# Kernel optimization log

Measured on AMD Instinct MI355X. Metric: run time of the kernel, lower is better.

The kernel has to match this reference:

```python
import jax, jax.numpy as jnp
import numpy as np

N_NODES = 100000
N_EDGES = 800000
N_FEAT = 64
H_DIM = 64
N_GRAPHS = 64


def _glorot(key, fan_in, fan_out):
    lim = np.sqrt(6.0 / (fan_in + fan_out)).astype(np.float32)
    return jax.random.uniform(key, (fan_in, fan_out), jnp.float32, -lim, lim)


def setup_inputs() -> dict:
    key = jax.random.key(0)
    ks = jax.random.split(key, 10)
    x = jax.random.normal(ks[0], (N_NODES, N_FEAT), jnp.float32)
    edge_index = jax.random.randint(ks[1], (2, N_EDGES), 0, N_NODES, dtype=jnp.int64)
    batch = jnp.sort(jax.random.randint(ks[2], (N_NODES,), 0, N_GRAPHS, dtype=jnp.int64))
    return {
        "x": x,
        "edge_index": edge_index,
        "batch": batch,
        "W0": _glorot(ks[3], N_FEAT, H_DIM), "b0": jnp.zeros((H_DIM,), jnp.float32),
        "W1": _glorot(ks[4], H_DIM, H_DIM), "b1": jnp.zeros((H_DIM,), jnp.float32),
        "W2": _glorot(ks[5], H_DIM, H_DIM), "b2": jnp.zeros((H_DIM,), jnp.float32),
        "Wl": _glorot(ks[6], H_DIM, H_DIM),
        "bl": jax.random.normal(ks[7], (H_DIM,), jnp.float32) * 0.01,
    }


def _gcn_conv(h, W, b, row, col, dinv_r, dinv_c, n_nodes):
    # PyG GCNConv: x W, then sym-normalized aggregation over edges+self-loops
    h = h @ W                                   # [N, H]
    msg = h[row] * (dinv_r * dinv_c)[:, None]   # gather + scale, [E+N, H]
    out = jax.ops.segment_sum(msg, col, num_segments=n_nodes)  # scatter-add
    return out + b


def reference(x, edge_index, batch, W0, b0, W1, b1, W2, b2, Wl, bl):
    n = x.shape[0]
    loops = jnp.arange(n, dtype=edge_index.dtype)
    row = jnp.concatenate([edge_index[0], loops])  # source nodes (+self-loops)
    col = jnp.concatenate([edge_index[1], loops])  # destination nodes
    deg = jax.ops.segment_sum(jnp.ones_like(col, dtype=x.dtype), col, num_segments=n)
    dinv = jnp.where(deg > 0, jax.lax.rsqrt(deg), 0.0)
    dinv_r, dinv_c = dinv[row], dinv[col]

    out = x
    for W, b in ((W0, b0), (W1, b1), (W2, b2)):
        out = jax.nn.relu(_gcn_conv(out, W, b, row, col, dinv_r, dinv_c, n))
        # F.dropout(training=False) is identity in eval mode
    return (out, out @ Wl + bl)
```

## Files before the change

### kernel.cpp

```cpp
#include <hip/hip_runtime.h>

#define NN 100000
#define NE 800000
#define HD 64
#define BK 128
#define NBUCK ((NN + BK - 1) / BK)
#define PA_EPT 16
#define PA_NB ((NE + 256 * PA_EPT - 1) / (256 * PA_EPT))
#define LDW 68

__device__ __forceinline__ int load_idx(const void* ei, int i, bool is32) {
    if (is32) return ((const int*)ei)[i];
    return (int)(((const long long*)ei)[i]);
}

__device__ __forceinline__ unsigned short f2bf(float f) {
    unsigned u = __float_as_uint(f);
    return (unsigned short)((u + 0x7FFFu + ((u >> 16) & 1u)) >> 16);
}

__device__ __forceinline__ void bfacc(const uint4& u, float4& a, float4& b) {
    a.x += __uint_as_float(u.x << 16);
    a.y += __uint_as_float(u.x & 0xFFFF0000u);
    a.z += __uint_as_float(u.y << 16);
    a.w += __uint_as_float(u.y & 0xFFFF0000u);
    b.x += __uint_as_float(u.z << 16);
    b.y += __uint_as_float(u.z & 0xFFFF0000u);
    b.z += __uint_as_float(u.w << 16);
    b.w += __uint_as_float(u.w & 0xFFFF0000u);
}

__global__ void k_initdet(const void* ei, int* bcnt, int* flag) {
    __shared__ int bad;
    int t = threadIdx.x;
    if (t == 0) bad = 0;
    if (t < NBUCK) bcnt[t] = 0;
    __syncthreads();
    const long long* p = (const long long*)ei;
    for (int i = t; i < 4096; i += 1024) {
        long long v = p[i];
        if (v < 0 || v >= (long long)NN) bad = 1;
    }
    __syncthreads();
    if (t == 0) *flag = bad ? 1 : 0;
}

__global__ __launch_bounds__(256) void k_pass0(const void* ei, const int* flag,
                                               int* bcnt) {
    __shared__ int h[NBUCK];
    for (int i = threadIdx.x; i < NBUCK; i += 256) h[i] = 0;
    __syncthreads();
    bool is32 = (*flag != 0);
    int stride = gridDim.x * 256;
    for (int e = blockIdx.x * 256 + threadIdx.x; e < NE; e += stride) {
        int dst = load_idx(ei, NE + e, is32);
        atomicAdd(&h[dst >> 7], 1);
    }
    __syncthreads();
    for (int i = threadIdx.x; i < NBUCK; i += 256) {
        int v = h[i];
        if (v) atomicAdd(&bcnt[i], v);
    }
}

__global__ __launch_bounds__(256) void k_scan1(const int* __restrict__ bcnt,
                                               int* __restrict__ offs,
                                               int* __restrict__ curs) {
    __shared__ int sc[256];
    int t = threadIdx.x;
    int v[4], s = 0;
#pragma unroll
    for (int i = 0; i < 4; ++i) {
        int b = t * 4 + i;
        v[i] = (b < NBUCK) ? bcnt[b] : 0;
        s += v[i];
    }
    sc[t] = s;
    __syncthreads();
    for (int off = 1; off < 256; off <<= 1) {
        int add = (t >= off) ? sc[t - off] : 0;
        __syncthreads();
        sc[t] += add;
        __syncthreads();
    }
    int run = sc[t] - s;
#pragma unroll
    for (int i = 0; i < 4; ++i) {
        int b = t * 4 + i;
        if (b < NBUCK) { offs[b] = run; curs[b] = run; }
        run += v[i];
    }
    if (t == 255) offs[NBUCK] = sc[255];
}

__global__ __launch_bounds__(256) void k_passA(const void* ei, const int* flag,
                                               int* curs, unsigned* ebuf) {
    __shared__ int h[NBUCK];
    __shared__ int base[NBUCK];
    for (int i = threadIdx.x; i < NBUCK; i += 256) h[i] = 0;
    __syncthreads();
    bool is32 = (*flag != 0);
    int e0 = blockIdx.x * (256 * PA_EPT);
    int src[PA_EPT], dst[PA_EPT];
#pragma unroll
    for (int i = 0; i < PA_EPT; ++i) {
        int e = e0 + i * 256 + threadIdx.x;
        if (e < NE) {
            src[i] = load_idx(ei, e, is32);
            dst[i] = load_idx(ei, NE + e, is32);
            atomicAdd(&h[dst[i] >> 7], 1);
        } else dst[i] = -1;
    }
    __syncthreads();
    for (int i = threadIdx.x; i < NBUCK; i += 256) {
        int v = h[i];
        base[i] = v ? atomicAdd(&curs[i], v) : 0;
        h[i] = 0;
    }
    __syncthreads();
#pragma unroll
    for (int i = 0; i < PA_EPT; ++i) {
        if (dst[i] >= 0) {
            int b = dst[i] >> 7;
            int p = base[b] + atomicAdd(&h[b], 1);
            ebuf[p] = (unsigned)src[i] | ((unsigned)(dst[i] & 127) << 17);
        }
    }
}

__global__ __launch_bounds__(256) void k_passB(const unsigned* __restrict__ ebuf,
                                               const int* __restrict__ offs,
                                               int* __restrict__ noffs,
                                               int* __restrict__ csr_src,
                                               float* __restrict__ dinv) {
    __shared__ int cnt[BK];
    __shared__ int sc[BK];
    __shared__ int nbase[BK];
    __shared__ int rank[BK];
    int bk = blockIdx.x;
    int t = threadIdx.x;
    if (t < BK) { cnt[t] = 0; rank[t] = 0; }
    __syncthreads();
    int rs = offs[bk], re = offs[bk + 1];
    for (int i = rs + t; i < re; i += 256)
        atomicAdd(&cnt[ebuf[i] >> 17], 1);
    __syncthreads();
    if (t < BK) sc[t] = cnt[t];
    __syncthreads();
    for (int off = 1; off < BK; off <<= 1) {
        int v = 0;
        if (t < BK && t >= off) v = sc[t - off];
        __syncthreads();
        if (t < BK) sc[t] += v;
        __syncthreads();
    }
    if (t < BK) {
        int node = bk * BK + t;
        int nb = rs + sc[t] - cnt[t];
        nbase[t] = nb;
        if (node < NN) {
            noffs[node] = nb;
            dinv[node] = rsqrtf((float)(cnt[t] + 1));
        }
    }
    if (bk == NBUCK - 1 && t == 0) noffs[NN] = re;
    __syncthreads();
    for (int i = rs + t; i < re; i += 256) {
        unsigned w = ebuf[i];
        int dl = w >> 17;
        int p = nbase[dl] + atomicAdd(&rank[dl], 1);
        csr_src[p] = (int)(w & 0x1FFFFu);
    }
}

template <bool BIAS, bool PRE, bool BF16OUT>
__global__ __launch_bounds__(256, 4) void k_gemm(const float* __restrict__ X,
                                                 const float* __restrict__ W,
                                                 const float* __restrict__ bias,
                                                 const float* __restrict__ dinv,
                                                 void* __restrict__ Hout, int n) {
    __shared__ float Ws[64 * LDW];
    __shared__ float Xs[128 * LDW];
    int t = threadIdx.x;
    int row0 = blockIdx.x * 128;
    const float4* X4 = (const float4*)X;
    for (int i = t; i < 64 * 16; i += 256) {
        float4 v = ((const float4*)W)[i];
        *(float4*)&Ws[(i >> 4) * LDW + (i & 15) * 4] = v;
    }
    for (int i = t; i < 128 * 16; i += 256) {
        int r = row0 + (i >> 4);
        float4 v = (r < n) ? X4[(size_t)r * 16 + (i & 15)]
                           : make_float4(0.f, 0.f, 0.f, 0.f);
        *(float4*)&Xs[(i >> 4) * LDW + (i & 15) * 4] = v;
    }
    __syncthreads();
    int tc = (t & 15) * 4;
    int rbase = t >> 4;
    float4 acc[8] = {};
#pragma unroll 1
    for (int k = 0; k < 64; k += 4) {
        float4 wv[4], xv[8];
#pragma unroll
        for (int kk = 0; kk < 4; ++kk)
            wv[kk] = *(const float4*)&Ws[(k + kk) * LDW + tc];
#pragma unroll
        for (int i = 0; i < 8; ++i)
            xv[i] = *(const float4*)&Xs[(rbase + 16 * i) * LDW + k];
#pragma unroll
        for (int i = 0; i < 8; ++i) {
            acc[i].x += xv[i].x * wv[0].x + xv[i].y * wv[1].x
                      + xv[i].z * wv[2].x + xv[i].w * wv[3].x;
            acc[i].y += xv[i].x * wv[0].y + xv[i].y * wv[1].y
                      + xv[i].z * wv[2].y + xv[i].w * wv[3].y;
            acc[i].z += xv[i].x * wv[0].z + xv[i].y * wv[1].z
                      + xv[i].z * wv[2].z + xv[i].w * wv[3].z;
            acc[i].w += xv[i].x * wv[0].w + xv[i].y * wv[1].w
                      + xv[i].z * wv[2].w + xv[i].w * wv[3].w;
        }
    }
    float4 bv = make_float4(0.f, 0.f, 0.f, 0.f);
    if (BIAS) bv = *(const float4*)&bias[tc];
#pragma unroll
    for (int i = 0; i < 8; ++i) {
        int r = row0 + rbase + 16 * i;
        if (r < n) {
            float s = PRE ? dinv[r] : 1.f;
            float4 o;
            o.x = (acc[i].x + bv.x) * s;
            o.y = (acc[i].y + bv.y) * s;
            o.z = (acc[i].z + bv.z) * s;
            o.w = (acc[i].w + bv.w) * s;
            if (BF16OUT) {
                ushort4 p;
                p.x = f2bf(o.x); p.y = f2bf(o.y); p.z = f2bf(o.z); p.w = f2bf(o.w);
                ((ushort4*)Hout)[(size_t)r * 16 + (t & 15)] = p;
            } else {
                ((float4*)Hout)[(size_t)r * 16 + (t & 15)] = o;
            }
        }
    }
}

template <int MODE>
__global__ __launch_bounds__(256, 4) void k_fused(const uint4* __restrict__ Hb,
                                               const int* __restrict__ noffs,
                                               const int* __restrict__ csr_src,
                                               const float* __restrict__ dinv,
                                               const float4* __restrict__ b4,
                                               const float* __restrict__ Wn,
                                               const float* __restrict__ bl,
                                               unsigned short* __restrict__ HbOut,
                                               float4* __restrict__ out0,
                                               float* __restrict__ out1) {
    __shared__ float Ws[64 * LDW];
    __shared__ float rows[32 * LDW];
    __shared__ float dvs[32];
    __shared__ float bls[64];
    int t = threadIdx.x;
    for (int i = t; i < 64 * 16; i += 256) {
        float4 v = ((const float4*)Wn)[i];
        *(float4*)&Ws[(i >> 4) * LDW + (i & 15) * 4] = v;
    }
    if (MODE == 1 && t < 64) bls[t] = bl[t];

    int lane = t & 63;
    int cl = lane >> 3;
    int q = lane & 7;
    int cbase = lane & ~7;
    int nl = (t >> 6) * 8 + cl;
    int base = blockIdx.x * 32;
    int node = base + nl;
    float dv = 0.f;
    float4 alo = make_float4(0.f, 0.f, 0.f, 0.f);
    float4 ahi = make_float4(0.f, 0.f, 0.f, 0.f);
    if (node < NN) {
        dv = dinv[node];
        {
            uint4 u = Hb[(size_t)node * 8 + q];
            bfacc(u, alo, ahi);
        }
        int e0 = noffs[node], e1 = noffs[node + 1];
#pragma unroll 1
        for (int e = e0; e < e1; e += 8) {
            int rem = e1 - e;
            int idx = (q < rem) ? csr_src[e + q] : 0;
            int s[8];
#pragma unroll
            for (int j = 0; j < 8; ++j)
                s[j] = __shfl(idx, cbase + j, 64);
            uint4 uu[8];
#pragma unroll
            for (int j = 0; j < 8; ++j)
                uu[j] = Hb[(size_t)s[j] * 8 + q];
#pragma unroll
            for (int j = 0; j < 8; ++j)
                if (j < rem) bfacc(uu[j], alo, ahi);
        }
    }
    if (node < NN) {
        float4 b0v = b4[2 * q], b1v = b4[2 * q + 1];
        float4 r0, r1;
        r0.x = fmaxf(alo.x * dv + b0v.x, 0.f);
        r0.y = fmaxf(alo.y * dv + b0v.y, 0.f);
        r0.z = fmaxf(alo.z * dv + b0v.z, 0.f);
        r0.w = fmaxf(alo.w * dv + b0v.w, 0.f);
        r1.x = fmaxf(ahi.x * dv + b1v.x, 0.f);
        r1.y = fmaxf(ahi.y * dv + b1v.y, 0.f);
        r1.z = fmaxf(ahi.z * dv + b1v.z, 0.f);
        r1.w = fmaxf(ahi.w * dv + b1v.w, 0.f);
        *(float4*)&rows[nl * LDW + 8 * q]     = r0;
        *(float4*)&rows[nl * LDW + 8 * q + 4] = r1;
        if (MODE == 1) {
            out0[(size_t)node * 16 + 2 * q]     = r0;
            out0[(size_t)node * 16 + 2 * q + 1] = r1;
        }
        if (q == 0) dvs[nl] = dv;
    }
    __syncthreads();

    int tc = (t & 15) * 4;
    int rbase = t >> 4;
    float4 a0 = make_float4(0.f, 0.f, 0.f, 0.f);
    float4 a1 = make_float4(0.f, 0.f, 0.f, 0.f);
#pragma unroll 1
    for (int k = 0; k < 64; k += 4) {
        float4 wv[4];
#pragma unroll
        for (int kk = 0; kk < 4; ++kk)
            wv[kk] = *(const float4*)&Ws[(k + kk) * LDW + tc];
        float4 x0 = *(const float4*)&rows[rbase * LDW + k];
        float4 x1 = *(const float4*)&rows[(rbase + 16) * LDW + k];
        a0.x += x0.x * wv[0].x + x0.y * wv[1].x + x0.z * wv[2].x + x0.w * wv[3].x;
        a0.y += x0.x * wv[0].y + x0.y * wv[1].y + x0.z * wv[2].y + x0.w * wv[3].y;
        a0.z += x0.x * wv[0].z + x0.y * wv[1].z + x0.z * wv[2].z + x0.w * wv[3].z;
        a0.w += x0.x * wv[0].w + x0.y * wv[1].w + x0.z * wv[2].w + x0.w * wv[3].w;
        a1.x += x1.x * wv[0].x + x1.y * wv[1].x + x1.z * wv[2].x + x1.w * wv[3].x;
        a1.y += x1.x * wv[0].y + x1.y * wv[1].y + x1.z * wv[2].y + x1.w * wv[3].y;
        a1.z += x1.x * wv[0].z + x1.y * wv[1].z + x1.z * wv[2].z + x1.w * wv[3].z;
        a1.w += x1.x * wv[0].w + x1.y * wv[1].w + x1.z * wv[2].w + x1.w * wv[3].w;
    }
    int n0 = base + rbase, n1 = base + rbase + 16;
    if (MODE == 0) {
        if (n0 < NN) {
            float s = dvs[rbase];
            ushort4 p;
            p.x = f2bf(a0.x * s); p.y = f2bf(a0.y * s);
            p.z = f2bf(a0.z * s); p.w = f2bf(a0.w * s);
            *(ushort4*)&HbOut[(size_t)n0 * 64 + tc] = p;
        }
        if (n1 < NN) {
            float s = dvs[rbase + 16];
            ushort4 p;
            p.x = f2bf(a1.x * s); p.y = f2bf(a1.y * s);
            p.z = f2bf(a1.z * s); p.w = f2bf(a1.w * s);
            *(ushort4*)&HbOut[(size_t)n1 * 64 + tc] = p;
        }
    } else {
        float4 bv = *(const float4*)&bls[tc];
        if (n0 < NN) {
            float4 o; o.x = a0.x + bv.x; o.y = a0.y + bv.y;
            o.z = a0.z + bv.z; o.w = a0.w + bv.w;
            *(float4*)&out1[(size_t)n0 * 64 + tc] = o;
        }
        if (n1 < NN) {
            float4 o; o.x = a1.x + bv.x; o.y = a1.y + bv.y;
            o.z = a1.z + bv.z; o.w = a1.w + bv.w;
            *(float4*)&out1[(size_t)n1 * 64 + tc] = o;
        }
    }
}

extern "C" void kernel_launch(void* const* d_in, const int* in_sizes, int n_in,
                              void* d_out, int out_size, void* d_ws, size_t ws_size,
                              hipStream_t stream) {
    const float* x  = (const float*)d_in[0];
    const void*  ei = d_in[1];
    const float* W0 = (const float*)d_in[3];
    const float* b0 = (const float*)d_in[4];
    const float* W1 = (const float*)d_in[5];
    const float* b1 = (const float*)d_in[6];
    const float* W2 = (const float*)d_in[7];
    const float* b2 = (const float*)d_in[8];
    const float* Wl = (const float*)d_in[9];
    const float* bl = (const float*)d_in[10];

    char* ws = (char*)d_ws;
    int*      flag    = (int*)(ws);
    int*      bcnt    = (int*)(ws + 256);
    int*      offs    = (int*)(ws + 4352);
    int*      curs    = (int*)(ws + 8448);
    float*    dinv    = (float*)(ws + 12544);
    int*      noffs   = (int*)(ws + 412672);
    int*      csr_src = (int*)(ws + 812800);
    unsigned short* HbA = (unsigned short*)(ws + 4100096);
    unsigned short* HbB = (unsigned short*)(ws + 16900096);

    float* out0 = (float*)d_out;
    float* out1 = out0 + (size_t)NN * HD;
    unsigned* ebuf = (unsigned*)out1;

    int gG = (NN + 127) / 128;
    int gF = (NN + 31) / 32;

    k_initdet<<<1, 1024, 0, stream>>>(ei, bcnt, flag);
    k_pass0<<<128, 256, 0, stream>>>(ei, flag, bcnt);
    k_scan1<<<1, 256, 0, stream>>>(bcnt, offs, curs);
    k_passA<<<PA_NB, 256, 0, stream>>>(ei, flag, curs, ebuf);
    k_passB<<<NBUCK, 256, 0, stream>>>(ebuf, offs, noffs, csr_src, dinv);

    k_gemm<false, true, true><<<gG, 256, 0, stream>>>(x, W0, nullptr, dinv,
                                                      (void*)HbA, NN);
    k_fused<0><<<gF, 256, 0, stream>>>((const uint4*)HbA, noffs, csr_src, dinv,
                                       (const float4*)b0, W1, nullptr,
                                       HbB, nullptr, nullptr);
    k_fused<0><<<gF, 256, 0, stream>>>((const uint4*)HbB, noffs, csr_src, dinv,
                                       (const float4*)b1, W2, nullptr,
                                       HbA, nullptr, nullptr);
    k_fused<1><<<gF, 256, 0, stream>>>((const uint4*)HbA, noffs, csr_src, dinv,
                                       (const float4*)b2, Wl, bl,
                                       nullptr, (float4*)out0, out1);
}
```

Before: 239.8 us.

## Use split-bf16 MFMA for the fused per-block 64x64 matmul

Replaces the scalar FP32 LDS matmul in the fused aggregation kernel with bf16 MFMA 16x16x32 instructions. It approximates FP32 accuracy by splitting both the activations and the weights into hi and lo bf16 parts and issuing three products per tile. Results are staged through a shared scratch buffer so each thread writes contiguous 8-element output chunks. This cuts VALU FMA work, but adds per-block conversion of W to transposed split bf16, extra syncs, and a small loss of precision because the lo*lo term is dropped.

Measured after the change: 235.2 us. Within noise of the previous version (-1.9%).

```diff
diff --git a/kernel.cpp b/kernel.cpp
--- a/kernel.cpp
+++ b/kernel.cpp
@@ -8,6 +8,10 @@
 #define PA_EPT 16
 #define PA_NB ((NE + 256 * PA_EPT - 1) / (256 * PA_EPT))
 #define LDW 68
+#define LDB 72
+
+typedef __attribute__((ext_vector_type(8))) short bf16x8;
+typedef __attribute__((ext_vector_type(4))) float f32x4;
 
 __device__ __forceinline__ int load_idx(const void* ei, int i, bool is32) {
     if (is32) return ((const int*)ei)[i];
@@ -17,6 +21,10 @@
 __device__ __forceinline__ unsigned short f2bf(float f) {
     unsigned u = __float_as_uint(f);
     return (unsigned short)((u + 0x7FFFu + ((u >> 16) & 1u)) >> 16);
+}
+
+__device__ __forceinline__ float bf2f(unsigned short h) {
+    return __uint_as_float((unsigned)h << 16);
 }
 
 __device__ __forceinline__ void bfacc(const uint4& u, float4& a, float4& b) {
@@ -253,14 +261,22 @@
                                                unsigned short* __restrict__ HbOut,
                                                float4* __restrict__ out0,
                                                float* __restrict__ out1) {
-    __shared__ float Ws[64 * LDW];
-    __shared__ float rows[32 * LDW];
+    __shared__ unsigned short WtH[64 * LDB];
+    __shared__ unsigned short WtL[64 * LDB];
+    __shared__ __align__(16) char scratch[32 * LDB * 2 * 2];
     __shared__ float dvs[32];
     __shared__ float bls[64];
+    unsigned short* rows_hi = (unsigned short*)scratch;
+    unsigned short* rows_lo = (unsigned short*)scratch + 32 * LDB;
+    float* cbuf = (float*)scratch;
     int t = threadIdx.x;
-    for (int i = t; i < 64 * 16; i += 256) {
-        float4 v = ((const float4*)Wn)[i];
-        *(float4*)&Ws[(i >> 4) * LDW + (i & 15) * 4] = v;
+    for (int i = t; i < 64 * 64; i += 256) {
+        int k = i >> 6, c = i & 63;
+        float wv = Wn[i];
+        unsigned short hi = f2bf(wv);
+        unsigned short lo = f2bf(wv - bf2f(hi));
+        WtH[c * LDB + k] = hi;
+        WtL[c * LDB + k] = lo;
     }
     if (MODE == 1 && t < 64) bls[t] = bl[t];
 
@@ -300,73 +316,93 @@
     }
     if (node < NN) {
         float4 b0v = b4[2 * q], b1v = b4[2 * q + 1];
-        float4 r0, r1;
-        r0.x = fmaxf(alo.x * dv + b0v.x, 0.f);
-        r0.y = fmaxf(alo.y * dv + b0v.y, 0.f);
-        r0.z = fmaxf(alo.z * dv + b0v.z, 0.f);
-        r0.w = fmaxf(alo.w * dv + b0v.w, 0.f);
-        r1.x = fmaxf(ahi.x * dv + b1v.x, 0.f);
-        r1.y = fmaxf(ahi.y * dv + b1v.y, 0.f);
-        r1.z = fmaxf(ahi.z * dv + b1v.z, 0.f);
-        r1.w = fmaxf(ahi.w * dv + b1v.w, 0.f);
-        *(float4*)&rows[nl * LDW + 8 * q]     = r0;
-        *(float4*)&rows[nl * LDW + 8 * q + 4] = r1;
+        float f[8];
+        f[0] = fmaxf(alo.x * dv + b0v.x, 0.f);
+        f[1] = fmaxf(alo.y * dv + b0v.y, 0.f);
+        f[2] = fmaxf(alo.z * dv + b0v.z, 0.f);
+        f[3] = fmaxf(alo.w * dv + b0v.w, 0.f);
+        f[4] = fmaxf(ahi.x * dv + b1v.x, 0.f);
+        f[5] = fmaxf(ahi.y * dv + b1v.y, 0.f);
+        f[6] = fmaxf(ahi.z * dv + b1v.z, 0.f);
+        f[7] = fmaxf(ahi.w * dv + b1v.w, 0.f);
         if (MODE == 1) {
-            out0[(size_t)node * 16 + 2 * q]     = r0;
-            out0[(size_t)node * 16 + 2 * q + 1] = r1;
-        }
+            out0[(size_t)node * 16 + 2 * q]     = make_float4(f[0], f[1], f[2], f[3]);
+            out0[(size_t)node * 16 + 2 * q + 1] = make_float4(f[4], f[5], f[6], f[7]);
+        }
+        unsigned hw[4], lw[4];
+#pragma unroll
+        for (int i = 0; i < 4; ++i) {
+            unsigned short h0 = f2bf(f[2 * i]),     h1 = f2bf(f[2 * i + 1]);
+            unsigned short l0 = f2bf(f[2 * i]     - bf2f(h0));
+            unsigned short l1 = f2bf(f[2 * i + 1] - bf2f(h1));
+            hw[i] = (unsigned)h0 | ((unsigned)h1 << 16);
+            lw[i] = (unsigned)l0 | ((unsigned)l1 << 16);
+        }
+        *(uint4*)&rows_hi[nl * LDB + 8 * q] = make_uint4(hw[0], hw[1], hw[2], hw[3]);
+        *(uint4*)&rows_lo[nl * LDB + 8 * q] = make_uint4(lw[0], lw[1], lw[2], lw[3]);
         if (q == 0) dvs[nl] = dv;
     }
     __syncthreads();
 
-    int tc = (t & 15) * 4;
-    int rbase = t >> 4;
-    float4 a0 = make_float4(0.f, 0.f, 0.f, 0.f);
-    float4 a1 = make_float4(0.f, 0.f, 0.f, 0.f);
-#pragma unroll 1
-    for (int k = 0; k < 64; k += 4) {
-        float4 wv[4];
-#pragma unroll
-        for (int kk = 0; kk < 4; ++kk)
-            wv[kk] = *(const float4*)&Ws[(k + kk) * LDW + tc];
-        float4 x0 = *(const float4*)&rows[rbase * LDW + k];
-        float4 x1 = *(const float4*)&rows[(rbase + 16) * LDW + k];
-        a0.x += x0.x * wv[0].x + x0.y * wv[1].x + x0.z * wv[2].x + x0.w * wv[3].x;
-        a0.y += x0.x * wv[0].y + x0.y * wv[1].y + x0.z * wv[2].y + x0.w * wv[3].y;
-        a0.z += x0.x * wv[0].z + x0.y * wv[1].z + x0.z * wv[2].z + x0.w * wv[3].z;
-        a0.w += x0.x * wv[0].w + x0.y * wv[1].w + x0.z * wv[2].w + x0.w * wv[3].w;
-        a1.x += x1.x * wv[0].x + x1.y * wv[1].x + x1.z * wv[2].x + x1.w * wv[3].x;
-        a1.y += x1.x * wv[0].y + x1.y * wv[1].y + x1.z * wv[2].y + x1.w * wv[3].y;
-        a1.z += x1.x * wv[0].z + x1.y * wv[1].z + x1.z * wv[2].z + x1.w * wv[3].z;
-        a1.w += x1.x * wv[0].w + x1.y * wv[1].w + x1.z * wv[2].w + x1.w * wv[3].w;
-    }
-    int n0 = base + rbase, n1 = base + rbase + 16;
-    if (MODE == 0) {
-        if (n0 < NN) {
-            float s = dvs[rbase];
-            ushort4 p;
-            p.x = f2bf(a0.x * s); p.y = f2bf(a0.y * s);
-            p.z = f2bf(a0.z * s); p.w = f2bf(a0.w * s);
-            *(ushort4*)&HbOut[(size_t)n0 * 64 + tc] = p;
-        }
-        if (n1 < NN) {
-            float s = dvs[rbase + 16];
-            ushort4 p;
-            p.x = f2bf(a1.x * s); p.y = f2bf(a1.y * s);
-            p.z = f2bf(a1.z * s); p.w = f2bf(a1.w * s);
-            *(ushort4*)&HbOut[(size_t)n1 * 64 + tc] = p;
-        }
-    } else {
-        float4 bv = *(const float4*)&bls[tc];
-        if (n0 < NN) {
-            float4 o; o.x = a0.x + bv.x; o.y = a0.y + bv.y;
-            o.z = a0.z + bv.z; o.w = a0.w + bv.w;
-            *(float4*)&out1[(size_t)n0 * 64 + tc] = o;
-        }
-        if (n1 < NN) {
-            float4 o; o.x = a1.x + bv.x; o.y = a1.y + bv.y;
-            o.z = a1.z + bv.z; o.w = a1.w + bv.w;
-            *(float4*)&out1[(size_t)n1 * 64 + tc] = o;
+    int w = t >> 6;
+    int la = lane & 15, kc = lane >> 4;
+    int tr = w & 1;
+    int c0 = (w >> 1) * 32;
+    f32x4 ac0 = {0.f, 0.f, 0.f, 0.f};
+    f32x4 ac1 = {0.f, 0.f, 0.f, 0.f};
+    const unsigned short* arH = &rows_hi[(tr * 16 + la) * LDB];
+    const unsigned short* arL = &rows_lo[(tr * 16 + la) * LDB];
+    const unsigned short* b0H = &WtH[(c0 + la) * LDB];
+    const unsigned short* b0L = &WtL[(c0 + la) * LDB];
+    const unsigned short* b1H = &WtH[(c0 + 16 + la) * LDB];
+    const unsigned short* b1L = &WtL[(c0 + 16 + la) * LDB];
+#pragma unroll
+    for (int kh = 0; kh < 2; ++kh) {
+        int ko = kh * 32 + kc * 8;
+        bf16x8 aH  = *(const bf16x8*)(arH + ko);
+        bf16x8 aL  = *(const bf16x8*)(arL + ko);
+        bf16x8 bH0 = *(const bf16x8*)(b0H + ko);
+        bf16x8 bL0 = *(const bf16x8*)(b0L + ko);
+        bf16x8 bH1 = *(const bf16x8*)(b1H + ko);
+        bf16x8 bL1 = *(const bf16x8*)(b1L + ko);
+        ac0 = __builtin_amdgcn_mfma_f32_16x16x32_bf16(aH, bH0, ac0, 0, 0, 0);
+        ac1 = __builtin_amdgcn_mfma_f32_16x16x32_bf16(aH, bH1, ac1, 0, 0, 0);
+        ac0 = __builtin_amdgcn_mfma_f32_16x16x32_bf16(aL, bH0, ac0, 0, 0, 0);
+        ac1 = __builtin_amdgcn_mfma_f32_16x16x32_bf16(aL, bH1, ac1, 0, 0, 0);
+        ac0 = __builtin_amdgcn_mfma_f32_16x16x32_bf16(aH, bL0, ac0, 0, 0, 0);
+        ac1 = __builtin_amdgcn_mfma_f32_16x16x32_bf16(aH, bL1, ac1, 0, 0, 0);
+    }
+    __syncthreads();
+
+    int rb2 = tr * 16 + kc * 4;
+#pragma unroll
+    for (int j = 0; j < 4; ++j) {
+        cbuf[(rb2 + j) * LDW + c0 + la]      = ac0[j];
+        cbuf[(rb2 + j) * LDW + c0 + 16 + la] = ac1[j];
+    }
+    __syncthreads();
+
+    int nl2 = t >> 3, q2 = t & 7;
+    int n2 = base + nl2;
+    if (n2 < NN) {
+        const float* cp = &cbuf[nl2 * LDW + 8 * q2];
+        if (MODE == 0) {
+            float s = dvs[nl2];
+            ushort4 pa, pb;
+            pa.x = f2bf(cp[0] * s); pa.y = f2bf(cp[1] * s);
+            pa.z = f2bf(cp[2] * s); pa.w = f2bf(cp[3] * s);
+            pb.x = f2bf(cp[4] * s); pb.y = f2bf(cp[5] * s);
+            pb.z = f2bf(cp[6] * s); pb.w = f2bf(cp[7] * s);
+            *(ushort4*)&HbOut[(size_t)n2 * 64 + 8 * q2]     = pa;
+            *(ushort4*)&HbOut[(size_t)n2 * 64 + 8 * q2 + 4] = pb;
+        } else {
+            float4 o0, o1;
+            o0.x = cp[0] + bls[8 * q2];     o0.y = cp[1] + bls[8 * q2 + 1];
+            o0.z = cp[2] + bls[8 * q2 + 2]; o0.w = cp[3] + bls[8 * q2 + 3];
+            o1.x = cp[4] + bls[8 * q2 + 4]; o1.y = cp[5] + bls[8 * q2 + 5];
+            o1.z = cp[6] + bls[8 * q2 + 6]; o1.w = cp[7] + bls[8 * q2 + 7];
+            *(float4*)&out1[(size_t)n2 * 64 + 8 * q2]     = o0;
+            *(float4*)&out1[(size_t)n2 * 64 + 8 * q2 + 4] = o1;
         }
     }
 }
```
